# Optimization experiments

Measured on AMD Instinct MI355X. Metric: run time of the kernel, lower is better.

The kernel has to match this reference:

```python
import jax, jax.numpy as jnp
import numpy as np

N = 100000          # nodes
E = 2000000         # edges
NUM_ET = 10         # num_edge_types
ED = 16             # edge_embedding_dim
LAYERS = [(64, 4, 16), (64, 4, 8)]  # (in_channels, heads, out_channels_per_head)
NEG_SLOPE = 0.2     # PyG GATConv default leaky_relu slope


def setup_inputs() -> dict:
    key = jax.random.key(0)
    ks = jax.random.split(key, 4 + 6 * len(LAYERS))
    inp = {
        "x": jax.random.normal(ks[0], (N, LAYERS[0][0]), jnp.float32),
        "edge_index": jax.random.randint(ks[1], (2, E), 0, N),
        "edge_type": jax.random.randint(ks[2], (E,), 0, NUM_ET),
        "edge_emb": jax.random.normal(ks[3], (NUM_ET, ED), jnp.float32) * 0.1,
    }
    k = 4
    for i, (cin, H, C) in enumerate(LAYERS):
        s = 1.0 / np.sqrt(cin)
        inp[f"l{i}_lin_w"] = jax.random.normal(ks[k], (H * C, cin), jnp.float32) * s; k += 1
        inp[f"l{i}_att_src"] = jax.random.normal(ks[k], (H, C), jnp.float32) * 0.1; k += 1
        inp[f"l{i}_att_dst"] = jax.random.normal(ks[k], (H, C), jnp.float32) * 0.1; k += 1
        inp[f"l{i}_lin_e_w"] = jax.random.normal(ks[k], (H * C, ED), jnp.float32) * (1.0 / np.sqrt(ED)); k += 1
        inp[f"l{i}_att_e"] = jax.random.normal(ks[k], (H, C), jnp.float32) * 0.1; k += 1
        inp[f"l{i}_bias"] = jnp.zeros((H * C,), jnp.float32); k += 1
    return inp


def gat_conv(x, src, dst, edge_attr, lin_w, a_src, a_dst, lin_e_w, a_e, bias, H, C):
    n = x.shape[0]
    h = (x @ lin_w.T).reshape(n, H, C)                 # [N,H,C]
    e = (edge_attr @ lin_e_w.T).reshape(-1, H, C)      # [E',H,C]
    s_src = jnp.einsum('nhc,hc->nh', h, a_src)
    s_dst = jnp.einsum('nhc,hc->nh', h, a_dst)
    alpha = s_src[src] + s_dst[dst] + jnp.einsum('ehc,hc->eh', e, a_e)  # [E',H]
    alpha = jax.nn.leaky_relu(alpha, NEG_SLOPE)
    # segment softmax over edges grouped by destination node
    amax = jax.ops.segment_max(alpha, dst, num_segments=n)
    ex = jnp.exp(alpha - amax[dst])
    denom = jax.ops.segment_sum(ex, dst, num_segments=n)
    w = ex / denom[dst]                                # [E',H]
    out = jax.ops.segment_sum(h[src] * w[..., None], dst, num_segments=n)
    return out.reshape(n, H * C) + bias


def reference(x, edge_index, edge_type, edge_emb,
              l0_lin_w, l0_att_src, l0_att_dst, l0_lin_e_w, l0_att_e, l0_bias,
              l1_lin_w, l1_att_src, l1_att_dst, l1_lin_e_w, l1_att_e, l1_bias):
    n = x.shape[0]
    edge_attr = edge_emb[edge_type]                    # [E,ED]
    # PyG GATConv default: add self-loops, fill their edge_attr with the mean
    loop = jnp.arange(n)
    src = jnp.concatenate([edge_index[0], loop])
    dst = jnp.concatenate([edge_index[1], loop])
    mean_attr = jnp.mean(edge_attr, axis=0)
    ea = jnp.concatenate([edge_attr, jnp.broadcast_to(mean_attr, (n, ED))], axis=0)

    h = gat_conv(x, src, dst, ea, l0_lin_w, l0_att_src, l0_att_dst,
                 l0_lin_e_w, l0_att_e, l0_bias, LAYERS[0][1], LAYERS[0][2])
    h = jax.nn.relu(h)  # dropout disabled (eval mode)
    out = gat_conv(h, src, dst, ea, l1_lin_w, l1_att_src, l1_att_dst,
                   l1_lin_e_w, l1_att_e, l1_bias, LAYERS[1][1], LAYERS[1][2])
    return out
```

## Files before the change

kernel.cpp:

```cpp
#include <hip/hip_runtime.h>
#include <hip/hip_fp16.h>
#include <cstdint>
#include <type_traits>

#define LRELU(a) ((a) > 0.f ? (a) : 0.2f * (a))
#define BBITS 9
#define BSZ   (1 << BBITS)
#define MAXB  256
#define SL    8
#define PSTR  12288
#define SLOT  48
#define SLOT4 (SLOT / 4)
#define LIDX(e) (((((e) >> 21) & (BSZ - 1)) * SL) + ((((e) & 131071)) >> 14))

typedef float cfloat4 __attribute__((ext_vector_type(4)));

__global__ __launch_bounds__(1024) void k13_scatter(
        const int* __restrict__ ei, const int* __restrict__ ety, int E,
        int* __restrict__ staging, int* __restrict__ bcnt, int* __restrict__ tcnt,
        int BSTRIDE) {
    __shared__ int ent[4096], ent2[4096];
    __shared__ unsigned char ebb[4096], ebb2[4096];
    __shared__ int lh[MAXB], lstart[MAXB], lcur[MAXB], sc[MAXB];
    __shared__ int lt[16];
    int t = threadIdx.x;
    if (t < 256) lh[t] = 0;
    if (t < 16) lt[t] = 0;
    __syncthreads();
    int base = blockIdx.x * 4096;
    int cnt = min(4096, E - base);
    for (int i = t; i < cnt; i += 1024) {
        int s = ei[base + i], d = ei[E + base + i], ty = ety[base + i];
        int b = d >> BBITS;
        ent[i] = s | (ty << 17) | ((d & (BSZ - 1)) << 21);
        ebb[i] = (unsigned char)b;
        atomicAdd(&lh[b], 1);
        atomicAdd(&lt[ty], 1);
    }
    __syncthreads();
    if (t < 256) sc[t] = lh[t];
    __syncthreads();
    for (int off = 1; off < 256; off <<= 1) {
        int a = (t >= off && t < 256) ? sc[t - off] : 0;
        __syncthreads();
        if (t < 256) sc[t] += a;
        __syncthreads();
    }
    if (t < 256) { lstart[t] = sc[t] - lh[t]; lcur[t] = lstart[t]; }
    __syncthreads();
    for (int i = t; i < cnt; i += 1024) {
        int b = ebb[i];
        int pos = atomicAdd(&lcur[b], 1);
        ent2[pos] = ent[i];
        ebb2[pos] = (unsigned char)b;
    }
    __syncthreads();
    for (int i = t; i < cnt; i += 1024) {
        int b = ebb2[i];
        int p = i - lstart[b];
        if (p < SLOT) staging[(size_t)b * BSTRIDE + blockIdx.x * SLOT + p] = ent2[i];
    }
    if (t < 256) bcnt[blockIdx.x * 256 + t] = lh[t];
    if (t < 16)  tcnt[blockIdx.x * 16 + t]  = lt[t];
}

template <int OUT, int C, typename XT>
__device__ void gemm_role(char* ldsbuf, int bid, const XT* __restrict__ x,
                          const float* __restrict__ W,
                          const float* __restrict__ asrc, const float* __restrict__ adst,
                          int N, __half* __restrict__ hout,
                          float* __restrict__ ssrc, float* __restrict__ sdst) {
    const int JG = OUT / 4;
    const int RG = 256 / JG;
    const int RPT = 64 / RG;
    const int WTP = OUT + 4;
    const int WQ = WTP / 4;
    float* xs = (float*)ldsbuf;
    cfloat4* wt4 = (cfloat4*)(ldsbuf + 64 * 68 * 4);
    float* wt = (float*)wt4;
    int t = threadIdx.x;
    for (int idx = t; idx < OUT * 64; idx += 256) {
        int j = idx >> 6, k = idx & 63;
        wt[k * WTP + j] = W[idx];
    }
    int rowbase = bid * 64;
    int nrows = min(64, N - rowbase);
    if constexpr (std::is_same<XT, float>::value) {
        const float4* px = (const float4*)x;
        for (int idx = t; idx < nrows * 16; idx += 256) {
            int r = idx >> 4, kq = idx & 15;
            float4 v = px[(size_t)(rowbase + r) * 16 + kq];
            float* dst = xs + r * 68 + kq * 4;
            dst[0] = v.x; dst[1] = v.y; dst[2] = v.z; dst[3] = v.w;
        }
    } else {
        const uint4* px = (const uint4*)x;
        for (int idx = t; idx < nrows * 8; idx += 256) {
            int r = idx >> 3, ko = idx & 7;
            uint4 u = px[(size_t)(rowbase + r) * 8 + ko];
            const __half2* hp = (const __half2*)&u;
            float* dst = xs + r * 68 + ko * 8;
#pragma unroll
            for (int i = 0; i < 4; ++i) {
                float2 f = __half22float2(hp[i]);
                dst[2 * i] = f.x;
                dst[2 * i + 1] = f.y;
            }
        }
    }
    if (nrows < 64)
        for (int idx = nrows * 64 + t; idx < 64 * 64; idx += 256)
            xs[(idx >> 6) * 68 + (idx & 63)] = 0.f;
    __syncthreads();
    int jg = t % JG, rg = t / JG;
    cfloat4 acc[RPT];
#pragma unroll
    for (int rr = 0; rr < RPT; ++rr) acc[rr] = cfloat4{0.f, 0.f, 0.f, 0.f};
    const float* xrow = xs + rg * RPT * 68;
#pragma unroll 4
    for (int k = 0; k < 64; ++k) {
        cfloat4 wv = wt4[k * WQ + jg];
#pragma unroll
        for (int rr = 0; rr < RPT; ++rr) acc[rr] += xrow[rr * 68 + k] * wv;
    }
    const int JH = C / 4;
    cfloat4 avs = ((const cfloat4*)asrc)[jg];
    cfloat4 avd = ((const cfloat4*)adst)[jg];
    int hd = jg / JH;
#pragma unroll
    for (int rr = 0; rr < RPT; ++rr) {
        int r = rg * RPT + rr;
        int row = rowbase + r;
        bool ok = r < nrows;
        if (ok) {
            ushort4 pk;
            pk.x = __half_as_ushort(__float2half(acc[rr][0]));
            pk.y = __half_as_ushort(__float2half(acc[rr][1]));
            pk.z = __half_as_ushort(__float2half(acc[rr][2]));
            pk.w = __half_as_ushort(__float2half(acc[rr][3]));
            *(ushort4*)(hout + (size_t)row * OUT + jg * 4) = pk;
        }
        float ps = acc[rr][0] * avs[0] + acc[rr][1] * avs[1] + acc[rr][2] * avs[2] + acc[rr][3] * avs[3];
        float pd = acc[rr][0] * avd[0] + acc[rr][1] * avd[1] + acc[rr][2] * avd[2] + acc[rr][3] * avd[3];
#pragma unroll
        for (int w = 1; w < JH; w <<= 1) {
            ps += __shfl_xor(ps, w);
            pd += __shfl_xor(pd, w);
        }
        if ((jg & (JH - 1)) == 0 && ok) {
            ssrc[row * 4 + hd] = ps;
            sdst[row * 4 + hd] = pd;
        }
    }
}

__device__ void k4_role(char* ldsbuf, int b, const int* __restrict__ staging,
                        const int* __restrict__ bcnt, int egrid, int BSTRIDE,
                        int N, int2* __restrict__ rowptr2, int* __restrict__ packed) {
    int* lcnt = (int*)ldsbuf;
    int* lcur = lcnt + BSZ * SL;
    int* tsum = lcur + BSZ * SL;
    int* cnts = tsum + 256;
    int t = threadIdx.x;
    int n0 = b << BBITS;
    for (int i = t; i < BSZ * SL; i += 256) lcnt[i] = 0;
    for (int k = t; k < 512; k += 256) cnts[k] = (k < egrid) ? min(bcnt[k * 256 + b], SLOT) : 0;
    __syncthreads();
    const int4* st4 = (const int4*)(staging + (size_t)b * BSTRIDE);
    int tot4 = egrid * SLOT4;
    for (int i = t; i < tot4; i += 256) {
        int k = i / SLOT4;
        int j0 = (i - k * SLOT4) * 4;
        int c = cnts[k];
        if (j0 < c) {
            int4 e4 = st4[i];
            int nv = c - j0;
            atomicAdd(&lcnt[LIDX(e4.x)], 1);
            if (nv > 1) atomicAdd(&lcnt[LIDX(e4.y)], 1);
            if (nv > 2) atomicAdd(&lcnt[LIDX(e4.z)], 1);
            if (nv > 3) atomicAdd(&lcnt[LIDX(e4.w)], 1);
        }
    }
    __syncthreads();
    int loc[2 * SL];
    int run = 0;
#pragma unroll
    for (int n = 0; n < 2; ++n)
#pragma unroll
        for (int j = 0; j < SL; ++j) {
            loc[n * SL + j] = run;
            run += lcnt[(2 * t + n) * SL + j];
        }
    tsum[t] = run;
    __syncthreads();
    for (int off = 1; off < 256; off <<= 1) {
        int a = (t >= off) ? tsum[t - off] : 0;
        __syncthreads();
        tsum[t] += a;
        __syncthreads();
    }
    int nbase = tsum[t] - run;
    int run0 = loc[SL];
    int node = n0 + 2 * t;
    int pbase = b * PSTR;
    if (node < N)     rowptr2[node]     = make_int2(pbase + nbase, pbase + nbase + run0);
    if (node + 1 < N) rowptr2[node + 1] = make_int2(pbase + nbase + run0, pbase + nbase + run);
#pragma unroll
    for (int n = 0; n < 2; ++n)
#pragma unroll
        for (int j = 0; j < SL; ++j) lcur[(2 * t + n) * SL + j] = nbase + loc[n * SL + j];
    __syncthreads();
    for (int i = t; i < tot4; i += 256) {
        int k = i / SLOT4;
        int j0 = (i - k * SLOT4) * 4;
        int c = cnts[k];
        if (j0 < c) {
            int4 e4 = st4[i];
            int nv = c - j0;
            int pos = atomicAdd(&lcur[LIDX(e4.x)], 1);
            if (pos < PSTR) packed[pbase + pos] = e4.x & 0x1FFFFF;
            if (nv > 1) {
                pos = atomicAdd(&lcur[LIDX(e4.y)], 1);
                if (pos < PSTR) packed[pbase + pos] = e4.y & 0x1FFFFF;
            }
            if (nv > 2) {
                pos = atomicAdd(&lcur[LIDX(e4.z)], 1);
                if (pos < PSTR) packed[pbase + pos] = e4.z & 0x1FFFFF;
            }
            if (nv > 3) {
                pos = atomicAdd(&lcur[LIDX(e4.w)], 1);
                if (pos < PSTR) packed[pbase + pos] = e4.w & 0x1FFFFF;
            }
        }
    }
}

__device__ void finalize_role(char* ldsbuf, const int* __restrict__ tcnt, int egrid, int E,
                              const float* __restrict__ emb,
                              const float* __restrict__ we0, const float* __restrict__ ae0,
                              const float* __restrict__ we1, const float* __restrict__ ae1,
                              float* __restrict__ alphaE) {
    int* part = (int*)ldsbuf;
    int* tot  = part + 256;
    float* tmp = (float*)(tot + 16);
    int t = threadIdx.x;
    int ty = t & 15, chunk = t >> 4;
    int s = 0;
    for (int k = chunk; k < egrid; k += 16) s += tcnt[k * 16 + ty];
    part[t] = s;
    __syncthreads();
    if (t < 16) {
        int v = 0;
        for (int p = 0; p < 16; ++p) v += part[p * 16 + t];
        tot[t] = v;
    }
    __syncthreads();
    if (t < 80) {
        int l = t / 40, r = t % 40, ty2 = r >> 2, h = r & 3;
        const float* w = l ? we1 : we0;
        const float* ae = l ? ae1 : ae0;
        int CC = l ? 8 : 16;
        const float* ev = emb + ty2 * 16;
        float val = 0.f;
        for (int c = 0; c < CC; ++c) {
            const float* wr = w + (h * CC + c) * 16;
            float s2 = 0.f;
            for (int d = 0; d < 16; ++d) s2 += wr[d] * ev[d];
            val += s2 * ae[h * CC + c];
        }
        tmp[l * 44 + ty2 * 4 + h] = val;
        alphaE[l * 44 + ty2 * 4 + h] = val;
    }
    __syncthreads();
    if (t < 8) {
        int l = t >> 2, h = t & 3;
        float s3 = 0.f;
        for (int ty3 = 0; ty3 < 10; ++ty3)
            s3 += (float)tot[ty3] * tmp[l * 44 + ty3 * 4 + h];
        alphaE[l * 44 + 40 + h] = s3 / (float)E;
    }
}

__global__ __launch_bounds__(256) void fused_gemm0_k4(
        int nK4, int nGemm,
        const float* __restrict__ x, const float* __restrict__ W,
        const float* __restrict__ asrc, const float* __restrict__ adst, int N,
        __half* __restrict__ hout, float* __restrict__ ssrc, float* __restrict__ sdst,
        const int* __restrict__ staging, const int* __restrict__ bcnt,
        int egrid, int BSTRIDE, int2* __restrict__ rowptr2, int* __restrict__ packed,
        const int* __restrict__ tcnt, int E,
        const float* __restrict__ emb,
        const float* __restrict__ we0, const float* __restrict__ ae0,
        const float* __restrict__ we1, const float* __restrict__ ae1,
        float* __restrict__ alphaE) {
    __shared__ __align__(16) char lds[35840];
    if (blockIdx.x < (unsigned)nK4)
        k4_role(lds, blockIdx.x, staging, bcnt, egrid, BSTRIDE, N, rowptr2, packed);
    else if (blockIdx.x < (unsigned)(nK4 + nGemm))
        gemm_role<64, 16, float>(lds, blockIdx.x - nK4, x, W, asrc, adst, N,
                                 hout, ssrc, sdst);
    else
        finalize_role(lds, tcnt, egrid, E, emb, we0, ae0, we1, ae1, alphaE);
}

__global__ __launch_bounds__(256) void gemmscore1(const __half* __restrict__ x,
                                                  const float* __restrict__ W,
                                                  const float* __restrict__ asrc,
                                                  const float* __restrict__ adst, int N,
                                                  __half* __restrict__ hout,
                                                  float* __restrict__ ssrc,
                                                  float* __restrict__ sdst) {
    __shared__ __align__(16) char lds[64 * 68 * 4 + 64 * 9 * 16];
    gemm_role<32, 8, __half>(lds, blockIdx.x, x, W, asrc, adst, N, hout, ssrc, sdst);
}

__device__ inline void fma_h8(float* acc, float4 v, float ex) {
    const __half2* h2 = (const __half2*)&v;
#pragma unroll
    for (int i = 0; i < 4; ++i) {
        float2 f = __half22float2(h2[i]);
        acc[2 * i]     += ex * f.x;
        acc[2 * i + 1] += ex * f.y;
    }
}

#define AGG_BODY(CUR, NXT, GI)                                                        \
    {                                                                                 \
        if ((GI) + 1 < np) {                                                          \
            _Pragma("unroll")                                                         \
            for (int e = 0; e < 4; ++e) {                                             \
                int n = pb##NXT[e] & 131071;                                          \
                sb##NXT[e] = ssrc[n * 4 + hd];                                        \
                ab##NXT[e] = aE[((pb##NXT[e] >> 17) & 15) * 4 + hd];                  \
                _Pragma("unroll")                                                     \
                for (int v = 0; v < VEC; ++v)                                         \
                    rb##NXT[e * VEC + v] =                                            \
                        *(const float4*)(hmat + (size_t)n * ROW + off + 8 * v);       \
            }                                                                         \
            if ((GI) + 2 < np) {                                                      \
                const int* pkn = pk + 4 * ((GI) + 2);                                 \
                _Pragma("unroll")                                                     \
                for (int e = 0; e < 4; ++e)                                           \
                    pb##CUR[e] = __builtin_nontemporal_load(&pkn[e]);                 \
            }                                                                         \
        }                                                                             \
        float a0 = LRELU(sb##CUR[0] + sd + ab##CUR[0]);                               \
        float a1 = LRELU(sb##CUR[1] + sd + ab##CUR[1]);                               \
        float a2 = LRELU(sb##CUR[2] + sd + ab##CUR[2]);                               \
        float a3 = LRELU(sb##CUR[3] + sd + ab##CUR[3]);                               \
        float mn = fmaxf(fmaxf(a0, a1), fmaxf(a2, a3));                               \
        float mnew = fmaxf(mn, m);                                                    \
        float rsc = __expf(m - mnew);                                                 \
        denom *= rsc;                                                                 \
        _Pragma("unroll")                                                             \
        for (int c = 0; c < CPT; ++c) acc[c] *= rsc;                                  \
        m = mnew;                                                                     \
        float e0 = __expf(a0 - m), e1 = __expf(a1 - m);                               \
        float e2 = __expf(a2 - m), e3 = __expf(a3 - m);                               \
        denom += (e0 + e1) + (e2 + e3);                                               \
        _Pragma("unroll")                                                             \
        for (int v = 0; v < VEC; ++v) {                                               \
            fma_h8(acc + 8 * v, rb##CUR[0 * VEC + v], e0);                            \
            fma_h8(acc + 8 * v, rb##CUR[1 * VEC + v], e1);                            \
            fma_h8(acc + 8 * v, rb##CUR[2 * VEC + v], e2);                            \
            fma_h8(acc + 8 * v, rb##CUR[3 * VEC + v], e3);                            \
        }                                                                             \
    }

template <int C, int TPN, bool RELU, typename OT>
__global__ __launch_bounds__(256) void agg_kernel(const int2* __restrict__ rp2,
                                                  const int* __restrict__ packed,
                                                  const __half* __restrict__ hmat,
                                                  const float* __restrict__ ssrc,
                                                  const float* __restrict__ sdst,
                                                  const float* __restrict__ alphaE,
                                                  const float* __restrict__ bias, int N,
                                                  OT* __restrict__ out) {
    const int HALVES = TPN / 4;
    const int CPT = 4 * C / TPN;
    const int VEC = CPT / 8;
    __shared__ float aE[44];
    if (threadIdx.x < 44) aE[threadIdx.x] = alphaE[threadIdx.x];
    __syncthreads();
    int t = blockIdx.x * 256 + threadIdx.x;
    if (t >= N * TPN) return;
    int node = t / TPN;
    int sub  = t % TPN;
    int hd   = sub / HALVES;
    int off  = hd * C + (sub % HALVES) * CPT;
    const int ROW = 4 * C;
    int2 be = rp2[node];
    int beg = be.x, end = be.y;
    float sd = sdst[node * 4 + hd];
    float m = LRELU(ssrc[node * 4 + hd] + sd + aE[40 + hd]);
    float denom = 1.f;
    float acc[CPT];
#pragma unroll
    for (int c = 0; c < CPT; ++c) acc[c] = 0.f;
#pragma unroll
    for (int v = 0; v < VEC; ++v) {
        float4 sv = *(const float4*)(hmat + (size_t)node * ROW + off + 8 * v);
        fma_h8(acc + 8 * v, sv, 1.f);
    }
    int np = (end - beg) >> 2;
    const int* pk = packed + beg;
    int pb0[4], pb1[4];
    float sb0[4], sb1[4], ab0[4], ab1[4];
    float4 rb0[4 * VEC], rb1[4 * VEC];
    if (np > 0) {
#pragma unroll
        for (int e = 0; e < 4; ++e) pb0[e] = __builtin_nontemporal_load(&pk[e]);
#pragma unroll
        for (int e = 0; e < 4; ++e) {
            int n = pb0[e] & 131071;
            sb0[e] = ssrc[n * 4 + hd];
            ab0[e] = aE[((pb0[e] >> 17) & 15) * 4 + hd];
#pragma unroll
            for (int v = 0; v < VEC; ++v)
                rb0[e * VEC + v] = *(const float4*)(hmat + (size_t)n * ROW + off + 8 * v);
        }
        if (np > 1) {
#pragma unroll
            for (int e = 0; e < 4; ++e) pb1[e] = __builtin_nontemporal_load(&pk[4 + e]);
        }
    }
    for (int gi = 0; gi < np; gi += 2) {
        AGG_BODY(0, 1, gi);
        if (gi + 1 < np) AGG_BODY(1, 0, gi + 1);
    }
    int k = beg + np * 4;
    for (; k < end; ++k) {
        int p0 = __builtin_nontemporal_load(&packed[k]);
        int n0 = p0 & 131071;
        float v0 = ssrc[n0 * 4 + hd];
        float4 r0[VEC];
#pragma unroll
        for (int v = 0; v < VEC; ++v)
            r0[v] = *(const float4*)(hmat + (size_t)n0 * ROW + off + 8 * v);
        float a0 = LRELU(v0 + sd + aE[((p0 >> 17) & 15) * 4 + hd]);
        float mnew = fmaxf(a0, m);
        float rsc = __expf(m - mnew);
        denom *= rsc;
#pragma unroll
        for (int c = 0; c < CPT; ++c) acc[c] *= rsc;
        m = mnew;
        float e0 = __expf(a0 - m);
        denom += e0;
#pragma unroll
        for (int v = 0; v < VEC; ++v) fma_h8(acc + 8 * v, r0[v], e0);
    }
    float inv = 1.f / denom;
    if constexpr (std::is_same<OT, __half>::value) {
#pragma unroll
        for (int v = 0; v < VEC; ++v) {
            union { cfloat4 vv; __half h[8]; } u;
#pragma unroll
            for (int c = 0; c < 8; ++c) {
                float a = fmaf(acc[8 * v + c], inv, bias[off + 8 * v + c]);
                if (RELU) a = fmaxf(a, 0.f);
                u.h[c] = __float2half(a);
            }
            cfloat4* op = (cfloat4*)(out + (size_t)node * ROW + off + 8 * v);
            __builtin_nontemporal_store(u.vv, op);
        }
    } else {
#pragma unroll
        for (int v = 0; v < VEC; ++v) {
            cfloat4 o0, o1;
#pragma unroll
            for (int c = 0; c < 4; ++c) {
                float a = fmaf(acc[8 * v + c], inv, bias[off + 8 * v + c]);
                float bq = fmaf(acc[8 * v + c + 4], inv, bias[off + 8 * v + c + 4]);
                if (RELU) { a = fmaxf(a, 0.f); bq = fmaxf(bq, 0.f); }
                o0[c] = a;
                o1[c] = bq;
            }
            cfloat4* op = (cfloat4*)(out + (size_t)node * ROW + off + 8 * v);
            __builtin_nontemporal_store(o0, op);
            __builtin_nontemporal_store(o1, op + 1);
        }
    }
}

extern "C" void kernel_launch(void* const* d_in, const int* in_sizes, int n_in,
                              void* d_out, int out_size, void* d_ws, size_t ws_size,
                              hipStream_t stream) {
    const float* x    = (const float*)d_in[0];
    const int*   ei   = (const int*)d_in[1];
    const int*   ety  = (const int*)d_in[2];
    const float* emb  = (const float*)d_in[3];
    const float* w0   = (const float*)d_in[4];
    const float* as0  = (const float*)d_in[5];
    const float* ad0  = (const float*)d_in[6];
    const float* we0  = (const float*)d_in[7];
    const float* ae0  = (const float*)d_in[8];
    const float* b0   = (const float*)d_in[9];
    const float* w1   = (const float*)d_in[10];
    const float* as1  = (const float*)d_in[11];
    const float* ad1  = (const float*)d_in[12];
    const float* we1  = (const float*)d_in[13];
    const float* ae1  = (const float*)d_in[14];
    const float* b1   = (const float*)d_in[15];

    const int N = in_sizes[0] / 64;
    const int E = in_sizes[1] / 2;
    const int NB = (N + BSZ - 1) >> BBITS;
    const int egrid = (E + 4095) / 4096;
    const int BSTRIDE = egrid * SLOT;

    char* ws = (char*)d_ws;
    size_t o = 0;
    auto alloc = [&](size_t bytes) { size_t r = o; o = (o + bytes + 255) & ~(size_t)255; return r; };
    size_t o_alphaE   = alloc(4 * 88);
    size_t o_bcnt     = alloc((size_t)4 * egrid * 256);
    size_t o_tcnt     = alloc((size_t)4 * egrid * 16);
    size_t o_rowptr2  = alloc((size_t)8 * N);
    size_t o_staging  = alloc((size_t)4 * NB * BSTRIDE);
    size_t o_packed   = alloc((size_t)4 * NB * PSTR);
    size_t o_h        = alloc((size_t)2 * N * 64);
    size_t o_x1h      = alloc((size_t)2 * N * 64);
    size_t o_ssrc     = alloc((size_t)4 * N * 4);
    size_t o_sdst     = alloc((size_t)4 * N * 4);
    (void)ws_size;

    float*  alphaE   = (float*)(ws + o_alphaE);
    int*    bcnt     = (int*)(ws + o_bcnt);
    int*    tcnt     = (int*)(ws + o_tcnt);
    int2*   rowptr2  = (int2*)(ws + o_rowptr2);
    int*    staging  = (int*)(ws + o_staging);
    int*    packed   = (int*)(ws + o_packed);
    __half* h0       = (__half*)(ws + o_h);
    __half* x1h      = (__half*)(ws + o_x1h);
    float*  ssrc     = (float*)(ws + o_ssrc);
    float*  sdst     = (float*)(ws + o_sdst);
    float*  outp     = (float*)d_out;

    int ggrid = (N + 63) / 64;

    k13_scatter<<<egrid, 1024, 0, stream>>>(ei, ety, E, staging, bcnt, tcnt, BSTRIDE);
    fused_gemm0_k4<<<NB + ggrid + 1, 256, 0, stream>>>(
        NB, ggrid, x, w0, as0, ad0, N, h0, ssrc, sdst,
        staging, bcnt, egrid, BSTRIDE, rowptr2, packed,
        tcnt, E, emb, we0, ae0, we1, ae1, alphaE);

    int agg_grid0 = (N * 4 + 255) / 256;
    int agg_grid1 = (N * 4 + 255) / 256;

    agg_kernel<16, 4, true, __half><<<agg_grid0, 256, 0, stream>>>(rowptr2, packed, h0,
                                                                   ssrc, sdst, alphaE,
                                                                   b0, N, x1h);
    gemmscore1<<<ggrid, 256, 0, stream>>>(x1h, w1, as1, ad1, N, h0, ssrc, sdst);
    agg_kernel<8, 4, false, float><<<agg_grid1, 256, 0, stream>>>(rowptr2, packed, h0,
                                                                  ssrc, sdst, alphaE + 44,
                                                                  b1, N, outp);
}
```

Baseline: 267.3 us.

## Degree-sort nodes per bucket for aggregation and simplify edge loop

```diff
diff --git a/kernel.cpp b/kernel.cpp
--- a/kernel.cpp
+++ b/kernel.cpp
@@ -156,15 +156,19 @@
 
 __device__ void k4_role(char* ldsbuf, int b, const int* __restrict__ staging,
                         const int* __restrict__ bcnt, int egrid, int BSTRIDE,
-                        int N, int2* __restrict__ rowptr2, int* __restrict__ packed) {
+                        int N, int2* __restrict__ rowptr2, int* __restrict__ packed,
+                        int* __restrict__ perm) {
     int* lcnt = (int*)ldsbuf;
     int* lcur = lcnt + BSZ * SL;
     int* tsum = lcur + BSZ * SL;
     int* cnts = tsum + 256;
+    int* hcnt = cnts + 512;
+    int* hoff = hcnt + 64;
     int t = threadIdx.x;
     int n0 = b << BBITS;
     for (int i = t; i < BSZ * SL; i += 256) lcnt[i] = 0;
     for (int k = t; k < 512; k += 256) cnts[k] = (k < egrid) ? min(bcnt[k * 256 + b], SLOT) : 0;
+    if (t < 64) hcnt[t] = 0;
     __syncthreads();
     const int4* st4 = (const int4*)(staging + (size_t)b * BSTRIDE);
     int tot4 = egrid * SLOT4;
@@ -205,11 +209,27 @@
     int pbase = b * PSTR;
     if (node < N)     rowptr2[node]     = make_int2(pbase + nbase, pbase + nbase + run0);
     if (node + 1 < N) rowptr2[node + 1] = make_int2(pbase + nbase + run0, pbase + nbase + run);
+    int key0 = min(run0, 63), key1 = min(run - run0, 63);
+    if (node < N)     atomicAdd(&hcnt[key0], 1);
+    if (node + 1 < N) atomicAdd(&hcnt[key1], 1);
 #pragma unroll
     for (int n = 0; n < 2; ++n)
 #pragma unroll
         for (int j = 0; j < SL; ++j) lcur[(2 * t + n) * SL + j] = nbase + loc[n * SL + j];
     __syncthreads();
+    if (t == 0) {
+        int runn = 0;
+        for (int k = 63; k >= 0; --k) { hoff[k] = runn; runn += hcnt[k]; }
+    }
+    __syncthreads();
+    if (node < N) {
+        int pos = atomicAdd(&hoff[key0], 1);
+        perm[(b << BBITS) + pos] = node;
+    }
+    if (node + 1 < N) {
+        int pos = atomicAdd(&hoff[key1], 1);
+        perm[(b << BBITS) + pos] = node + 1;
+    }
     for (int i = t; i < tot4; i += 256) {
         int k = i / SLOT4;
         int j0 = (i - k * SLOT4) * 4;
@@ -288,14 +308,15 @@
         __half* __restrict__ hout, float* __restrict__ ssrc, float* __restrict__ sdst,
         const int* __restrict__ staging, const int* __restrict__ bcnt,
         int egrid, int BSTRIDE, int2* __restrict__ rowptr2, int* __restrict__ packed,
+        int* __restrict__ perm,
         const int* __restrict__ tcnt, int E,
         const float* __restrict__ emb,
         const float* __restrict__ we0, const float* __restrict__ ae0,
         const float* __restrict__ we1, const float* __restrict__ ae1,
         float* __restrict__ alphaE) {
-    __shared__ __align__(16) char lds[35840];
+    __shared__ __align__(16) char lds[36352];
     if (blockIdx.x < (unsigned)nK4)
-        k4_role(lds, blockIdx.x, staging, bcnt, egrid, BSTRIDE, N, rowptr2, packed);
+        k4_role(lds, blockIdx.x, staging, bcnt, egrid, BSTRIDE, N, rowptr2, packed, perm);
     else if (blockIdx.x < (unsigned)(nK4 + nGemm))
         gemm_role<64, 16, float>(lds, blockIdx.x - nK4, x, W, asrc, adst, N,
                                  hout, ssrc, sdst);
@@ -324,49 +345,6 @@
     }
 }
 
-#define AGG_BODY(CUR, NXT, GI)                                                        \
-    {                                                                                 \
-        if ((GI) + 1 < np) {                                                          \
-            _Pragma("unroll")                                                         \
-            for (int e = 0; e < 4; ++e) {                                             \
-                int n = pb##NXT[e] & 131071;                                          \
-                sb##NXT[e] = ssrc[n * 4 + hd];                                        \
-                ab##NXT[e] = aE[((pb##NXT[e] >> 17) & 15) * 4 + hd];                  \
-                _Pragma("unroll")                                                     \
-                for (int v = 0; v < VEC; ++v)                                         \
-                    rb##NXT[e * VEC + v] =                                            \
-                        *(const float4*)(hmat + (size_t)n * ROW + off + 8 * v);       \
-            }                                                                         \
-            if ((GI) + 2 < np) {                                                      \
-                const int* pkn = pk + 4 * ((GI) + 2);                                 \
-                _Pragma("unroll")                                                     \
-                for (int e = 0; e < 4; ++e)                                           \
-                    pb##CUR[e] = __builtin_nontemporal_load(&pkn[e]);                 \
-            }                                                                         \
-        }                                                                             \
-        float a0 = LRELU(sb##CUR[0] + sd + ab##CUR[0]);                               \
-        float a1 = LRELU(sb##CUR[1] + sd + ab##CUR[1]);                               \
-        float a2 = LRELU(sb##CUR[2] + sd + ab##CUR[2]);                               \
-        float a3 = LRELU(sb##CUR[3] + sd + ab##CUR[3]);                               \
-        float mn = fmaxf(fmaxf(a0, a1), fmaxf(a2, a3));                               \
-        float mnew = fmaxf(mn, m);                                                    \
-        float rsc = __expf(m - mnew);                                                 \
-        denom *= rsc;                                                                 \
-        _Pragma("unroll")                                                             \
-        for (int c = 0; c < CPT; ++c) acc[c] *= rsc;                                  \
-        m = mnew;                                                                     \
-        float e0 = __expf(a0 - m), e1 = __expf(a1 - m);                               \
-        float e2 = __expf(a2 - m), e3 = __expf(a3 - m);                               \
-        denom += (e0 + e1) + (e2 + e3);                                               \
-        _Pragma("unroll")                                                             \
-        for (int v = 0; v < VEC; ++v) {                                               \
-            fma_h8(acc + 8 * v, rb##CUR[0 * VEC + v], e0);                            \
-            fma_h8(acc + 8 * v, rb##CUR[1 * VEC + v], e1);                            \
-            fma_h8(acc + 8 * v, rb##CUR[2 * VEC + v], e2);                            \
-            fma_h8(acc + 8 * v, rb##CUR[3 * VEC + v], e3);                            \
-        }                                                                             \
-    }
-
 template <int C, int TPN, bool RELU, typename OT>
 __global__ __launch_bounds__(256) void agg_kernel(const int2* __restrict__ rp2,
                                                   const int* __restrict__ packed,
@@ -374,7 +352,8 @@
                                                   const float* __restrict__ ssrc,
                                                   const float* __restrict__ sdst,
                                                   const float* __restrict__ alphaE,
-                                                  const float* __restrict__ bias, int N,
+                                                  const float* __restrict__ bias,
+                                                  const int* __restrict__ perm, int N,
                                                   OT* __restrict__ out) {
     const int HALVES = TPN / 4;
     const int CPT = 4 * C / TPN;
@@ -383,8 +362,9 @@
     if (threadIdx.x < 44) aE[threadIdx.x] = alphaE[threadIdx.x];
     __syncthreads();
     int t = blockIdx.x * 256 + threadIdx.x;
-    if (t >= N * TPN) return;
-    int node = t / TPN;
+    int g = t / TPN;
+    if (g >= N) return;
+    int node = perm[g];
     int sub  = t % TPN;
     int hd   = sub / HALVES;
     int off  = hd * C + (sub % HALVES) * CPT;
@@ -402,33 +382,46 @@
         float4 sv = *(const float4*)(hmat + (size_t)node * ROW + off + 8 * v);
         fma_h8(acc + 8 * v, sv, 1.f);
     }
-    int np = (end - beg) >> 2;
-    const int* pk = packed + beg;
-    int pb0[4], pb1[4];
-    float sb0[4], sb1[4], ab0[4], ab1[4];
-    float4 rb0[4 * VEC], rb1[4 * VEC];
-    if (np > 0) {
-#pragma unroll
-        for (int e = 0; e < 4; ++e) pb0[e] = __builtin_nontemporal_load(&pk[e]);
-#pragma unroll
-        for (int e = 0; e < 4; ++e) {
-            int n = pb0[e] & 131071;
-            sb0[e] = ssrc[n * 4 + hd];
-            ab0[e] = aE[((pb0[e] >> 17) & 15) * 4 + hd];
-#pragma unroll
-            for (int v = 0; v < VEC; ++v)
-                rb0[e * VEC + v] = *(const float4*)(hmat + (size_t)n * ROW + off + 8 * v);
-        }
-        if (np > 1) {
-#pragma unroll
-            for (int e = 0; e < 4; ++e) pb1[e] = __builtin_nontemporal_load(&pk[4 + e]);
-        }
-    }
-    for (int gi = 0; gi < np; gi += 2) {
-        AGG_BODY(0, 1, gi);
-        if (gi + 1 < np) AGG_BODY(1, 0, gi + 1);
-    }
-    int k = beg + np * 4;
+    int k = beg;
+    for (; k + 4 <= end; k += 4) {
+        int p0 = __builtin_nontemporal_load(&packed[k]);
+        int p1 = __builtin_nontemporal_load(&packed[k + 1]);
+        int p2 = __builtin_nontemporal_load(&packed[k + 2]);
+        int p3 = __builtin_nontemporal_load(&packed[k + 3]);
+        int n0 = p0 & 131071, n1 = p1 & 131071, n2 = p2 & 131071, n3 = p3 & 131071;
+        float v0 = ssrc[n0 * 4 + hd], v1 = ssrc[n1 * 4 + hd];
+        float v2 = ssrc[n2 * 4 + hd], v3 = ssrc[n3 * 4 + hd];
+        float4 r0[VEC], r1[VEC], r2[VEC], r3[VEC];
+#pragma unroll
+        for (int v = 0; v < VEC; ++v) {
+            r0[v] = *(const float4*)(hmat + (size_t)n0 * ROW + off + 8 * v);
+            r1[v] = *(const float4*)(hmat + (size_t)n1 * ROW + off + 8 * v);
+            r2[v] = *(const float4*)(hmat + (size_t)n2 * ROW + off + 8 * v);
+            r3[v] = *(const float4*)(hmat + (size_t)n3 * ROW + off + 8 * v);
+        }
+        float a0 = LRELU(v0 + sd + aE[((p0 >> 17) & 15) * 4 + hd]);
+        float a1 = LRELU(v1 + sd + aE[((p1 >> 17) & 15) * 4 + hd]);
+        float a2 = LRELU(v2 + sd + aE[((p2 >> 17) & 15) * 4 + hd]);
+        float a3 = LRELU(v3 + sd + aE[((p3 >> 17) & 15) * 4 + hd]);
+        float mn = fmaxf(fmaxf(a0, a1), fmaxf(a2, a3));
+        if (mn > m) {
+            float r = __expf(m - mn);
+            denom *= r;
+#pragma unroll
+            for (int c = 0; c < CPT; ++c) acc[c] *= r;
+            m = mn;
+        }
+        float e0 = __expf(a0 - m), e1 = __expf(a1 - m);
+        float e2 = __expf(a2 - m), e3 = __expf(a3 - m);
+        denom += (e0 + e1) + (e2 + e3);
+#pragma unroll
+        for (int v = 0; v < VEC; ++v) {
+            fma_h8(acc + 8 * v, r0[v], e0);
+            fma_h8(acc + 8 * v, r1[v], e1);
+            fma_h8(acc + 8 * v, r2[v], e2);
+            fma_h8(acc + 8 * v, r3[v], e3);
+        }
+    }
     for (; k < end; ++k) {
         int p0 = __builtin_nontemporal_load(&packed[k]);
         int n0 = p0 & 131071;
@@ -438,12 +431,13 @@
         for (int v = 0; v < VEC; ++v)
             r0[v] = *(const float4*)(hmat + (size_t)n0 * ROW + off + 8 * v);
         float a0 = LRELU(v0 + sd + aE[((p0 >> 17) & 15) * 4 + hd]);
-        float mnew = fmaxf(a0, m);
-        float rsc = __expf(m - mnew);
-        denom *= rsc;
-#pragma unroll
-        for (int c = 0; c < CPT; ++c) acc[c] *= rsc;
-        m = mnew;
+        if (a0 > m) {
+            float r = __expf(m - a0);
+            denom *= r;
+#pragma unroll
+            for (int c = 0; c < CPT; ++c) acc[c] *= r;
+            m = a0;
+        }
         float e0 = __expf(a0 - m);
         denom += e0;
 #pragma unroll
@@ -515,6 +509,7 @@
     size_t o_bcnt     = alloc((size_t)4 * egrid * 256);
     size_t o_tcnt     = alloc((size_t)4 * egrid * 16);
     size_t o_rowptr2  = alloc((size_t)8 * N);
+    size_t o_perm     = alloc((size_t)4 * NB * BSZ);
     size_t o_staging  = alloc((size_t)4 * NB * BSTRIDE);
     size_t o_packed   = alloc((size_t)4 * NB * PSTR);
     size_t o_h        = alloc((size_t)2 * N * 64);
@@ -527,6 +522,7 @@
     int*    bcnt     = (int*)(ws + o_bcnt);
     int*    tcnt     = (int*)(ws + o_tcnt);
     int2*   rowptr2  = (int2*)(ws + o_rowptr2);
+    int*    perm     = (int*)(ws + o_perm);
     int*    staging  = (int*)(ws + o_staging);
     int*    packed   = (int*)(ws + o_packed);
     __half* h0       = (__half*)(ws + o_h);
@@ -540,17 +536,16 @@
     k13_scatter<<<egrid, 1024, 0, stream>>>(ei, ety, E, staging, bcnt, tcnt, BSTRIDE);
     fused_gemm0_k4<<<NB + ggrid + 1, 256, 0, stream>>>(
         NB, ggrid, x, w0, as0, ad0, N, h0, ssrc, sdst,
-        staging, bcnt, egrid, BSTRIDE, rowptr2, packed,
+        staging, bcnt, egrid, BSTRIDE, rowptr2, packed, perm,
         tcnt, E, emb, we0, ae0, we1, ae1, alphaE);
 
-    int agg_grid0 = (N * 4 + 255) / 256;
-    int agg_grid1 = (N * 4 + 255) / 256;
-
-    agg_kernel<16, 4, true, __half><<<agg_grid0, 256, 0, stream>>>(rowptr2, packed, h0,
-                                                                   ssrc, sdst, alphaE,
-                                                                   b0, N, x1h);
+    int agg_grid = (NB * BSZ * 4 + 255) / 256;
+
+    agg_kernel<16, 4, true, __half><<<agg_grid, 256, 0, stream>>>(rowptr2, packed, h0,
+                                                                  ssrc, sdst, alphaE,
+                                                                  b0, perm, N, x1h);
     gemmscore1<<<ggrid, 256, 0, stream>>>(x1h, w1, as1, ad1, N, h0, ssrc, sdst);
-    agg_kernel<8, 4, false, float><<<agg_grid1, 256, 0, stream>>>(rowptr2, packed, h0,
-                                                                  ssrc, sdst, alphaE + 44,
-                                                                  b1, N, outp);
-}
+    agg_kernel<8, 4, false, float><<<agg_grid, 256, 0, stream>>>(rowptr2, packed, h0,
+                                                                 ssrc, sdst, alphaE + 44,
+                                                                 b1, perm, N, outp);
+}
```

Result: slower. 302.7 us (+13.3%).
